# Performance work log

Hardware: AMD Instinct MI355X
Metric: run time of the kernel (lower is better)

The kernel has to match this reference:

```python
import jax, jax.numpy as jnp
import numpy as np

INPUTSIZE = 40
K = 5          # kenrnal_size
STRIDE = 3
KN = 32        # kenrnal_num
LABEL_NODES = 50
BATCH = 64
SAMPLE_NUM = 4


def _build_model():
    """Replicates __init__/create_J_H: dense symmetric Ising coupling J and field H."""
    starts = np.arange(0, INPUTSIZE - K + 1, STRIDE)          # window starts (torch unfold)
    win = starts[:, None] + np.arange(K)                      # [P, K] pixel rows/cols per window
    P = win.shape[0]
    # image_idxs[p] = flattened pixel indices of patch p (row-major over H windows then W windows)
    image_idxs = (win[:, None, :, None] * INPUTSIZE + win[None, :, None, :]).reshape(P * P, K * K)
    cnn_idxs = np.tile(image_idxs, (KN, 1))                   # [cnn_n, K*K]
    cnn_flags = np.repeat(np.arange(KN), P * P)               # kernel id per cnn node

    img_n = INPUTSIZE * INPUTSIZE
    cnn_n = cnn_idxs.shape[0]
    out_n = LABEL_NODES
    N = img_n + cnn_n + out_n

    rng = np.random.default_rng(0)
    J_CNN = (rng.standard_normal((KN, K * K)) * 0.01).astype(np.float32)
    J_MLP = (rng.standard_normal((cnn_n, out_n)) * 0.01).astype(np.float32)
    H = np.concatenate([
        rng.standard_normal(img_n) * 0.01,
        np.zeros(cnn_n),
        rng.standard_normal(out_n) * 0.01,
    ]).astype(np.float32)

    J = np.zeros((N, N), np.float32)
    rows = img_n + np.repeat(np.arange(cnn_n), K * K)
    cols = cnn_idxs.reshape(-1)
    vals = J_CNN[cnn_flags].reshape(-1)
    J[rows, cols] = vals
    J[cols, rows] = vals
    J[img_n:img_n + cnn_n, img_n + cnn_n:] = J_MLP
    J[img_n + cnn_n:, img_n:img_n + cnn_n] = J_MLP.T

    # Graph is bipartite (edges only cnn<->img and cnn<->out): valid 2-coloring.
    group1 = np.arange(img_n, img_n + cnn_n, dtype=np.int64)                      # cnn nodes
    group0 = np.concatenate([np.arange(img_n, dtype=np.int64),
                             np.arange(img_n + cnn_n, N, dtype=np.int64)])        # img + output nodes
    return J, H, group0, group1


def setup_inputs() -> dict:
    J, H, group0, group1 = _build_model()
    key = jax.random.key(0)
    # create_m: random +/-1 spins
    m = jnp.where(jax.random.randint(key, (BATCH, J.shape[0]), 0, 2) == 0, -1.0, 1.0).astype(jnp.float32)
    return {
        "m": m,
        "J": jnp.asarray(J),
        "H": jnp.asarray(H),
        "group0": jnp.asarray(group0),
        "group1": jnp.asarray(group1),
        "sample_num": SAMPLE_NUM,
    }


def reference(m, J, H, group0, group1, sample_num):
    """construct(): sample_num sweeps of per-color-group Gibbs updates.
    Per group: I = J[idxs] @ m.T + H[idxs]; m[:, idxs] = sign(tanh(I) - U(-1,1)).
    """
    keys = jax.random.split(jax.random.key(1), int(sample_num))

    def sweep(m, k):
        k0, k1 = jax.random.split(k)
        for idxs, kk in ((group0, k0), (group1, k1)):
            I = m @ J[idxs].T + H[idxs]                       # [B, |group|]
            u = jax.random.uniform(kk, I.shape, dtype=I.dtype) * 2.0 - 1.0
            m = m.at[:, idxs].set(jnp.sign(jnp.tanh(I) - u))
        return m, None

    m, _ = jax.lax.scan(sweep, m, keys)
    return m


if __name__ == "__main__":
    out = reference(**setup_inputs())
    print(out.shape, out.dtype)
```

## Files before the change

kernel.cpp:

```cpp
#include <hip/hip_runtime.h>
#include <stdint.h>

#define NN     6258
#define IMG_N  1600
#define CNN_N  4608
#define OUT_N  50
#define BATCH  64
#define G0SZ   1650
#define G1SZ   4608
#define IMGW   40
#define NPATCH 12

__host__ __device__ inline void tf2x32(uint32_t k0, uint32_t k1,
                                       uint32_t x0, uint32_t x1,
                                       uint32_t& o0, uint32_t& o1) {
    uint32_t ks[3] = {k0, k1, k0 ^ k1 ^ 0x1BD11BDAu};
    const int rotA[4] = {13, 15, 26, 6};
    const int rotB[4] = {17, 29, 16, 24};
    x0 += ks[0];
    x1 += ks[1];
#pragma unroll
    for (int i = 0; i < 5; ++i) {
        const int* rot = (i & 1) ? rotB : rotA;
#pragma unroll
        for (int j = 0; j < 4; ++j) {
            x0 += x1;
            x1 = (x1 << rot[j]) | (x1 >> (32 - rot[j]));
            x1 ^= x0;
        }
        x0 += ks[(i + 1) % 3];
        x1 += ks[(i + 2) % 3] + (uint32_t)(i + 1);
    }
    o0 = x0;
    o1 = x1;
}

__device__ inline float jax_uniform_pm1(uint32_t k0, uint32_t k1, uint32_t j) {
    uint32_t o0, o1;
    tf2x32(k0, k1, 0u, j, o0, o1);
    uint32_t bits = o0 ^ o1;
    float f = __uint_as_float((bits >> 9) | 0x3f800000u);
    return (f - 1.0f) * 2.0f - 1.0f;
}

__device__ inline float tanh_xla_f32(float x) {
    if (fabsf(x) < 0.0004f) return x;
    float xc = fminf(fmaxf(x, -9.0f), 9.0f);
    float x2 = __fmul_rn(xc, xc);
    float num = -2.76076847742355e-16f;
    num = __fadd_rn(__fmul_rn(num, x2), 2.00018790482477e-13f);
    num = __fadd_rn(__fmul_rn(num, x2), -8.60467152213735e-11f);
    num = __fadd_rn(__fmul_rn(num, x2), 5.12229709037114e-08f);
    num = __fadd_rn(__fmul_rn(num, x2), 1.48572235717979e-05f);
    num = __fadd_rn(__fmul_rn(num, x2), 6.37261928875436e-04f);
    num = __fadd_rn(__fmul_rn(num, x2), 4.89352455891786e-03f);
    num = __fmul_rn(num, xc);
    float den = 1.19825839466702e-06f;
    den = __fadd_rn(__fmul_rn(den, x2), 1.18534705686654e-04f);
    den = __fadd_rn(__fmul_rn(den, x2), 2.26843463243900e-03f);
    den = __fadd_rn(__fmul_rn(den, x2), 4.89352518554385e-03f);
    return __fdiv_rn(num, den);
}

__device__ inline float gibbs_decide(double acc, float h, float u) {
    float I32 = (float)(acc + (double)h);
    float t = tanh_xla_f32(I32);
    float d = __fadd_rn(t, -u);
    return (d > 0.0f) ? 1.0f : ((d < 0.0f) ? -1.0f : 0.0f);
}

__global__ __launch_bounds__(256) void g0_kernel(float* __restrict__ m,
                                                 const float* __restrict__ J,
                                                 const float* __restrict__ H,
                                                 uint32_t k0, uint32_t k1) {
    int blk = blockIdx.x;
    if (blk < 400) {
        int tid = blk * 256 + (int)threadIdx.x;
        int g = tid >> 6;
        int b = tid & 63;
        int r = g / IMGW, c = g % IMGW;
        int pr_lo = (r >= 4) ? (r - 2) / 3 : 0;
        int pr_hi = r / 3; if (pr_hi > NPATCH - 1) pr_hi = NPATCH - 1;
        int pc_lo = (c >= 4) ? (c - 2) / 3 : 0;
        int pc_hi = c / 3; if (pc_hi > NPATCH - 1) pc_hi = NPATCH - 1;
        const float* Jrow = J + (size_t)g * NN;
        const float* mrow = m + (size_t)b * NN;
        double acc = 0.0;
        for (int pr = pr_lo; pr <= pr_hi; ++pr) {
            for (int pc = pc_lo; pc <= pc_hi; ++pc) {
                int base = IMG_N + pr * NPATCH + pc;
#pragma unroll
                for (int f = 0; f < 32; ++f) {
                    int col = base + f * 144;
                    acc += (double)Jrow[col] * (double)mrow[col];
                }
            }
        }
        float u = jax_uniform_pm1(k0, k1, (uint32_t)(b * G0SZ + g));
        m[(size_t)b * NN + g] = gibbs_decide(acc, H[g], u);
    } else {
        int w = (blk - 400) * 4 + ((int)threadIdx.x >> 6);
        int lane = (int)threadIdx.x & 63;
        int o = w >> 6;
        int b = w & 63;
        const float* Jrow = J + (size_t)(IMG_N + CNN_N + o) * NN + IMG_N;
        const float* mrow = m + (size_t)b * NN + IMG_N;
        double acc = 0.0;
        for (int k = lane; k < CNN_N; k += 64)
            acc += (double)Jrow[k] * (double)mrow[k];
        for (int off = 32; off >= 1; off >>= 1)
            acc += __shfl_xor(acc, off, 64);
        if (lane == 0) {
            float u = jax_uniform_pm1(k0, k1, (uint32_t)(b * G0SZ + IMG_N + o));
            m[(size_t)b * NN + IMG_N + CNN_N + o] =
                gibbs_decide(acc, H[IMG_N + CNN_N + o], u);
        }
    }
}

__global__ __launch_bounds__(256) void g1_kernel(float* __restrict__ m,
                                                 const float* __restrict__ J,
                                                 const float* __restrict__ H,
                                                 uint32_t k0, uint32_t k1) {
    int tid = blockIdx.x * 256 + (int)threadIdx.x;
    int cnode = tid >> 6;
    int b = tid & 63;
    int p = cnode % 144;
    int pr = p / NPATCH, pc = p % NPATCH;
    int r0 = pr * 3, c0 = pc * 3;
    const float* Jrow = J + (size_t)(IMG_N + cnode) * NN;
    const float* mrow = m + (size_t)b * NN;
    double acc = 0.0;
#pragma unroll
    for (int a = 0; a < 5; ++a) {
        int rowbase = (r0 + a) * IMGW + c0;
#pragma unroll
        for (int bb = 0; bb < 5; ++bb) {
            int pix = rowbase + bb;
            acc += (double)Jrow[pix] * (double)mrow[pix];
        }
    }
    const float* Jo = Jrow + IMG_N + CNN_N;
    const float* mo = mrow + IMG_N + CNN_N;
    for (int o = 0; o < OUT_N; ++o)
        acc += (double)Jo[o] * (double)mo[o];
    float u = jax_uniform_pm1(k0, k1, (uint32_t)(b * G1SZ + cnode));
    m[(size_t)b * NN + IMG_N + cnode] = gibbs_decide(acc, H[IMG_N + cnode], u);
}

extern "C" void kernel_launch(void* const* d_in, const int* in_sizes, int n_in,
                              void* d_out, int out_size, void* d_ws, size_t ws_size,
                              hipStream_t stream) {
    const float* m_in = (const float*)d_in[0];
    const float* J    = (const float*)d_in[1];
    const float* H    = (const float*)d_in[2];
    float* m = (float*)d_out;

    hipMemcpyAsync(m, m_in, sizeof(float) * (size_t)BATCH * NN,
                   hipMemcpyDeviceToDevice, stream);

    uint32_t K[4][2];
    for (int i = 0; i < 4; ++i)
        tf2x32(0u, 1u, 0u, (uint32_t)i, K[i][0], K[i][1]);

    for (int s = 0; s < 4; ++s) {
        uint32_t k0a, k0b, k1a, k1b;
        tf2x32(K[s][0], K[s][1], 0u, 0u, k0a, k0b);
        tf2x32(K[s][0], K[s][1], 0u, 1u, k1a, k1b);
        g0_kernel<<<1200, 256, 0, stream>>>(m, J, H, k0a, k0b);
        g1_kernel<<<1152, 256, 0, stream>>>(m, J, H, k1a, k1b);
    }
}
```

Measured before the change: 438.2 us.

## Store spin state node-major in workspace for coalesced batch-lane access

The spin matrix is transposed into a node-major [NN][64] workspace, so the 64 batch lanes of a wavefront read consecutive addresses instead of addresses strided by NN. The output-node reduction is reorganized so each block handles one output node, with four waves splitting the CNN range and combining partial sums through shared memory. This costs an extra transpose kernel at the start and at the end, and it changes the floating-point summation order for the output nodes.

```diff
diff --git a/kernel.cpp b/kernel.cpp
--- a/kernel.cpp
+++ b/kernel.cpp
@@ -69,10 +69,29 @@
     return (d > 0.0f) ? 1.0f : ((d < 0.0f) ? -1.0f : 0.0f);
 }
 
-__global__ __launch_bounds__(256) void g0_kernel(float* __restrict__ m,
+__global__ __launch_bounds__(256) void t_in(const float* __restrict__ src,
+                                            float* __restrict__ dst) {
+    int tid = blockIdx.x * 256 + (int)threadIdx.x;
+    if (tid < NN * BATCH) {
+        int node = tid >> 6, b = tid & 63;
+        dst[tid] = src[(size_t)b * NN + node];
+    }
+}
+
+__global__ __launch_bounds__(256) void t_out(const float* __restrict__ src,
+                                             float* __restrict__ dst) {
+    int tid = blockIdx.x * 256 + (int)threadIdx.x;
+    if (tid < NN * BATCH) {
+        int b = tid / NN, node = tid - b * NN;
+        dst[tid] = src[node * 64 + b];
+    }
+}
+
+__global__ __launch_bounds__(256) void g0_kernel(float* __restrict__ mt,
                                                  const float* __restrict__ J,
                                                  const float* __restrict__ H,
                                                  uint32_t k0, uint32_t k1) {
+    __shared__ double red[4][64];
     int blk = blockIdx.x;
     if (blk < 400) {
         int tid = blk * 256 + (int)threadIdx.x;
@@ -84,7 +103,6 @@
         int pc_lo = (c >= 4) ? (c - 2) / 3 : 0;
         int pc_hi = c / 3; if (pc_hi > NPATCH - 1) pc_hi = NPATCH - 1;
         const float* Jrow = J + (size_t)g * NN;
-        const float* mrow = m + (size_t)b * NN;
         double acc = 0.0;
         for (int pr = pr_lo; pr <= pr_hi; ++pr) {
             for (int pc = pc_lo; pc <= pc_hi; ++pc) {
@@ -92,33 +110,34 @@
 #pragma unroll
                 for (int f = 0; f < 32; ++f) {
                     int col = base + f * 144;
-                    acc += (double)Jrow[col] * (double)mrow[col];
+                    acc += (double)Jrow[col] * (double)mt[col * 64 + b];
                 }
             }
         }
         float u = jax_uniform_pm1(k0, k1, (uint32_t)(b * G0SZ + g));
-        m[(size_t)b * NN + g] = gibbs_decide(acc, H[g], u);
+        mt[g * 64 + b] = gibbs_decide(acc, H[g], u);
     } else {
-        int w = (blk - 400) * 4 + ((int)threadIdx.x >> 6);
+        int o = blk - 400;
+        int w = (int)threadIdx.x >> 6;
         int lane = (int)threadIdx.x & 63;
-        int o = w >> 6;
-        int b = w & 63;
         const float* Jrow = J + (size_t)(IMG_N + CNN_N + o) * NN + IMG_N;
-        const float* mrow = m + (size_t)b * NN + IMG_N;
         double acc = 0.0;
-        for (int k = lane; k < CNN_N; k += 64)
-            acc += (double)Jrow[k] * (double)mrow[k];
-        for (int off = 32; off >= 1; off >>= 1)
-            acc += __shfl_xor(acc, off, 64);
-        if (lane == 0) {
-            float u = jax_uniform_pm1(k0, k1, (uint32_t)(b * G0SZ + IMG_N + o));
-            m[(size_t)b * NN + IMG_N + CNN_N + o] =
-                gibbs_decide(acc, H[IMG_N + CNN_N + o], u);
+        int k0i = w * 1152, k1i = k0i + 1152;
+#pragma unroll 4
+        for (int k = k0i; k < k1i; ++k)
+            acc += (double)Jrow[k] * (double)mt[(IMG_N + k) * 64 + lane];
+        red[w][lane] = acc;
+        __syncthreads();
+        if (w == 0) {
+            double a = ((red[0][lane] + red[1][lane]) + red[2][lane]) + red[3][lane];
+            float u = jax_uniform_pm1(k0, k1, (uint32_t)(lane * G0SZ + IMG_N + o));
+            mt[(IMG_N + CNN_N + o) * 64 + lane] =
+                gibbs_decide(a, H[IMG_N + CNN_N + o], u);
         }
     }
 }
 
-__global__ __launch_bounds__(256) void g1_kernel(float* __restrict__ m,
+__global__ __launch_bounds__(256) void g1_kernel(float* __restrict__ mt,
                                                  const float* __restrict__ J,
                                                  const float* __restrict__ H,
                                                  uint32_t k0, uint32_t k1) {
@@ -129,7 +148,6 @@
     int pr = p / NPATCH, pc = p % NPATCH;
     int r0 = pr * 3, c0 = pc * 3;
     const float* Jrow = J + (size_t)(IMG_N + cnode) * NN;
-    const float* mrow = m + (size_t)b * NN;
     double acc = 0.0;
 #pragma unroll
     for (int a = 0; a < 5; ++a) {
@@ -137,15 +155,15 @@
 #pragma unroll
         for (int bb = 0; bb < 5; ++bb) {
             int pix = rowbase + bb;
-            acc += (double)Jrow[pix] * (double)mrow[pix];
+            acc += (double)Jrow[pix] * (double)mt[pix * 64 + b];
         }
     }
     const float* Jo = Jrow + IMG_N + CNN_N;
-    const float* mo = mrow + IMG_N + CNN_N;
+#pragma unroll 10
     for (int o = 0; o < OUT_N; ++o)
-        acc += (double)Jo[o] * (double)mo[o];
+        acc += (double)Jo[o] * (double)mt[(IMG_N + CNN_N + o) * 64 + b];
     float u = jax_uniform_pm1(k0, k1, (uint32_t)(b * G1SZ + cnode));
-    m[(size_t)b * NN + IMG_N + cnode] = gibbs_decide(acc, H[IMG_N + cnode], u);
+    mt[(IMG_N + cnode) * 64 + b] = gibbs_decide(acc, H[IMG_N + cnode], u);
 }
 
 extern "C" void kernel_launch(void* const* d_in, const int* in_sizes, int n_in,
@@ -154,10 +172,11 @@
     const float* m_in = (const float*)d_in[0];
     const float* J    = (const float*)d_in[1];
     const float* H    = (const float*)d_in[2];
-    float* m = (float*)d_out;
+    float* m_out = (float*)d_out;
+    float* mt    = (float*)d_ws;
 
-    hipMemcpyAsync(m, m_in, sizeof(float) * (size_t)BATCH * NN,
-                   hipMemcpyDeviceToDevice, stream);
+    const int TN = (NN * BATCH + 255) / 256;
+    t_in<<<TN, 256, 0, stream>>>(m_in, mt);
 
     uint32_t K[4][2];
     for (int i = 0; i < 4; ++i)
@@ -167,7 +186,9 @@
         uint32_t k0a, k0b, k1a, k1b;
         tf2x32(K[s][0], K[s][1], 0u, 0u, k0a, k0b);
         tf2x32(K[s][0], K[s][1], 0u, 1u, k1a, k1b);
-        g0_kernel<<<1200, 256, 0, stream>>>(m, J, H, k0a, k0b);
-        g1_kernel<<<1152, 256, 0, stream>>>(m, J, H, k1a, k1b);
+        g0_kernel<<<450, 256, 0, stream>>>(mt, J, H, k0a, k0b);
+        g1_kernel<<<1152, 256, 0, stream>>>(mt, J, H, k1a, k1b);
     }
+
+    t_out<<<TN, 256, 0, stream>>>(mt, m_out);
 }
```

New measurement: 528.0 us. +20.5%, slower.
